# Kernel tuning notes

Hardware: AMD Instinct MI355X
Metric: run time of the kernel (lower is better)

## Reference

```python
import jax, jax.numpy as jnp
import numpy as np

N = 50000      # batch_node_num (unique nodes)
E = 800000     # number of edges (avg degree 16)
IN = 128       # in_dim
OUT = 128      # out_dim
B = 10000      # query nodes


def setup_inputs() -> dict:
    key = jax.random.key(0)
    k = jax.random.split(key, 8)
    edges = jax.random.randint(k[0], (E, 2), 0, N, dtype=jnp.int64)
    node_idx = jax.random.randint(k[1], (B,), 0, N, dtype=jnp.int64)
    local_features = jax.random.normal(k[2], (N, IN), dtype=jnp.float32)
    W1 = jax.random.normal(k[3], (IN, OUT), dtype=jnp.float32) * (1.0 / np.sqrt(IN))
    b1 = jnp.zeros((OUT,), dtype=jnp.float32)
    W2 = jax.random.normal(k[4], (OUT, OUT), dtype=jnp.float32) * (1.0 / np.sqrt(OUT))
    b2 = jnp.zeros((OUT,), dtype=jnp.float32)
    return {"edges": edges, "node_idx": node_idx, "local_features": local_features,
            "W1": W1, "b1": b1, "W2": W2, "b2": b2, "ind": 2}


def reference(edges, node_idx, local_features, W1, b1, W2, b2, ind):
    mask = jnp.array([1.0, 1.0, 0.0, 0.0], dtype=jnp.float32)
    # Linear -> Tanh -> Linear (the out_linear_layer MLP)
    h = jnp.tanh(local_features @ W1 + b1) @ W2 + b2          # [N, OUT]
    src, dst = edges[:, 0], edges[:, 1]
    # self-loop edges get weight mask[ind], others weight 1
    values = jnp.where(src == dst, mask[ind], jnp.float32(1.0))  # [E]
    # spmm(matrix, ones) == per-row degree (weighted)
    row_sum = jax.ops.segment_sum(values, src, num_segments=N)   # [N]
    row_sum = jnp.where(row_sum == 0, jnp.float32(1.0), row_sum)
    # spmm(matrix, new_embeddings): gather dst embeddings, scatter-add to src
    results = jax.ops.segment_sum(values[:, None] * h[dst], src, num_segments=N)  # [N, OUT]
    output_emb = results / row_sum[:, None]
    return output_emb[node_idx]
```

## Files before the change

kernel.cpp:

```cpp
#include <hip/hip_runtime.h>

#define IN_DIM 128
#define CAP 128
#define LDT 136
#define SCAT_BLOCKS 377

typedef short v8s __attribute__((ext_vector_type(8)));
typedef float v4f __attribute__((ext_vector_type(4)));

__device__ inline unsigned short f2bf(float f) {
    unsigned int u = __float_as_uint(f);
    u += 0x7FFFu + ((u >> 16) & 1u);
    return (unsigned short)(u >> 16);
}
__device__ inline float bf2f(unsigned short h) {
    return __uint_as_float((unsigned int)h << 16);
}
__device__ inline float fast_tanh(float x) {
    float e = __builtin_amdgcn_exp2f(x * 2.885390081777927f);
    return 1.0f - 2.0f * __builtin_amdgcn_rcpf(e + 1.0f);
}

__global__ __launch_bounds__(256) void prep(
    const float* __restrict__ W1, const float* __restrict__ W2,
    unsigned short* __restrict__ Wf1, unsigned short* __restrict__ Wf2,
    const int* __restrict__ node_idx, int* __restrict__ flag, int B,
    int* __restrict__ cursor, int N, int nbF)
{
    int bid = blockIdx.x;
    if (bid < 128) {
        int i = bid * 256 + threadIdx.x;
        int m = i >> 14, o = i & 16383;
        int j   = o & 7;
        int l15 = (o >> 3) & 15;
        int quad = (o >> 7) & 3;
        int ct  = (o >> 9) & 7;
        int kk  = (o >> 12) & 3;
        int k = kk * 32 + quad * 8 + j;
        int n = ct * 16 + l15;
        float wv = (m ? W2 : W1)[k * 128 + n];
        (m ? Wf2 : Wf1)[o] = f2bf(wv);
    } else if (bid < 128 + nbF) {
        int i = (bid - 128) * 256 + threadIdx.x;
        if (i < B) flag[node_idx[i]] = 1;
    } else {
        int i = (bid - 128 - nbF) * 256 + threadIdx.x;
        if (i < N) cursor[i] = 0;
    }
}

__global__ __launch_bounds__(256, 3) void mlp_fill(
    const float* __restrict__ X,
    const unsigned short* __restrict__ Wf1, const unsigned short* __restrict__ Wf2,
    const float* __restrict__ b1, const float* __restrict__ b2,
    unsigned short* __restrict__ Hb, int nrows,
    const int* __restrict__ edges, const int* __restrict__ flag,
    const int* __restrict__ indp, int* __restrict__ cursor,
    unsigned short* __restrict__ col, int E, int mlpBlocks)
{
    const int bid = blockIdx.x;

    if (bid >= mlpBlocks) {
        const int keepSelf = (*indp < 2) ? 1 : 0;
        const int stride = SCAT_BLOCKS * 256;
        for (int e = (bid - mlpBlocks) * 256 + threadIdx.x; e < E; e += stride) {
            int2 ed = ((const int2*)edges)[e];
            if ((ed.x != ed.y || keepSelf) && flag[ed.x] == 1) {
                int p = atomicAdd(&cursor[ed.x], 1);
                if (p < CAP)
                    col[(size_t)ed.x * CAP + p] = (unsigned short)ed.y;
            }
        }
        return;
    }

    __shared__ unsigned short Ts[4 * 32 * LDT];
    const int t    = threadIdx.x;
    const int w    = t >> 6;
    const int lane = t & 63;
    const int l15  = lane & 15;
    const int quad = lane >> 4;
    const int R0   = bid * 128;
    const int wrow = w * 32;
    unsigned short* Tw = &Ts[w * 32 * LDT];

    int gr0 = R0 + wrow + l15;        gr0 = gr0 < nrows ? gr0 : nrows - 1;
    int gr1 = R0 + wrow + 16 + l15;   gr1 = gr1 < nrows ? gr1 : nrows - 1;
    const float* xrow[2] = { &X[(size_t)gr0 * 128 + quad * 8],
                             &X[(size_t)gr1 * 128 + quad * 8] };

    const v8s* Wp1 = (const v8s*)Wf1 + lane;
    const v8s* Wp2 = (const v8s*)Wf2 + lane;

    v4f acc[2][8];
#pragma unroll
    for (int rt = 0; rt < 2; ++rt)
#pragma unroll
        for (int ct = 0; ct < 8; ++ct)
            acc[rt][ct] = (v4f){0.f, 0.f, 0.f, 0.f};

#pragma unroll
    for (int kk = 0; kk < 4; ++kk) {
        v8s Ar[2];
#pragma unroll
        for (int rt = 0; rt < 2; ++rt) {
            const float* xp = xrow[rt] + kk * 32;
            float4 x0 = *(const float4*)xp;
            float4 x1 = *(const float4*)(xp + 4);
            v8s av;
            av[0] = (short)f2bf(x0.x); av[1] = (short)f2bf(x0.y);
            av[2] = (short)f2bf(x0.z); av[3] = (short)f2bf(x0.w);
            av[4] = (short)f2bf(x1.x); av[5] = (short)f2bf(x1.y);
            av[6] = (short)f2bf(x1.z); av[7] = (short)f2bf(x1.w);
            Ar[rt] = av;
        }
#pragma unroll
        for (int ct = 0; ct < 8; ++ct) {
            v8s Bfc = Wp1[(kk * 8 + ct) * 64];
            acc[0][ct] = __builtin_amdgcn_mfma_f32_16x16x32_bf16(
                Ar[0], Bfc, acc[0][ct], 0, 0, 0);
            acc[1][ct] = __builtin_amdgcn_mfma_f32_16x16x32_bf16(
                Ar[1], Bfc, acc[1][ct], 0, 0, 0);
        }
    }
#pragma unroll
    for (int ct = 0; ct < 8; ++ct) {
        float bias = b1[ct * 16 + l15];
#pragma unroll
        for (int rt = 0; rt < 2; ++rt) {
#pragma unroll
            for (int r = 0; r < 4; ++r)
                Tw[(rt * 16 + quad * 4 + r) * LDT + ct * 16 + l15] =
                    f2bf(fast_tanh(acc[rt][ct][r] + bias));
            acc[rt][ct] = (v4f){0.f, 0.f, 0.f, 0.f};
        }
    }


#pragma unroll
    for (int kk = 0; kk < 4; ++kk) {
        v8s Ar[2];
#pragma unroll
        for (int rt = 0; rt < 2; ++rt)
            Ar[rt] = *(const v8s*)
                &Tw[(rt * 16 + l15) * LDT + kk * 32 + quad * 8];
#pragma unroll
        for (int ct = 0; ct < 8; ++ct) {
            v8s Bfc = Wp2[(kk * 8 + ct) * 64];
            acc[0][ct] = __builtin_amdgcn_mfma_f32_16x16x32_bf16(
                Ar[0], Bfc, acc[0][ct], 0, 0, 0);
            acc[1][ct] = __builtin_amdgcn_mfma_f32_16x16x32_bf16(
                Ar[1], Bfc, acc[1][ct], 0, 0, 0);
        }
    }
    asm volatile("s_waitcnt lgkmcnt(0)" ::: "memory");
#pragma unroll
    for (int ct = 0; ct < 8; ++ct) {
        float bias = b2[ct * 16 + l15];
#pragma unroll
        for (int rt = 0; rt < 2; ++rt)
#pragma unroll
            for (int r = 0; r < 4; ++r)
                Tw[(rt * 16 + quad * 4 + r) * LDT + ct * 16 + l15] =
                    f2bf(acc[rt][ct][r] + bias);
    }
    asm volatile("s_waitcnt lgkmcnt(0)" ::: "memory");
#pragma unroll
    for (int i = 0; i < 8; ++i) {
        int lr = i * 4 + quad;
        int c  = l15;
        uint4 v = *(const uint4*)&Tw[lr * LDT + c * 8];
        int grow = R0 + wrow + lr;
        if (grow < nrows)
            *(uint4*)&Hb[(size_t)grow * 128 + c * 8] = v;
    }
}

__global__ __launch_bounds__(256) void aggregate_out(
    const int* __restrict__ node_idx, const int* __restrict__ cursor,
    const unsigned short* __restrict__ col, const unsigned short* __restrict__ Hb,
    float* __restrict__ out, int B)
{
    int b = (int)((blockIdx.x * blockDim.x + threadIdx.x) >> 6);
    if (b >= B) return;
    int lane = threadIdx.x & 63;
    int v = __builtin_amdgcn_readfirstlane(node_idx[b]);
    int deg = cursor[v];
    deg = deg < CAP ? deg : CAP;
    const unsigned short* cp = &col[(size_t)v * CAP];

    float sx[4] = {0.f, 0.f, 0.f, 0.f};
    float sy[4] = {0.f, 0.f, 0.f, 0.f};
    for (int c0 = 0; c0 < deg; c0 += 16) {
        unsigned int u[16];
#pragma unroll
        for (int k = 0; k < 16; ++k) {
            int idx = c0 + k;
            idx = idx < deg ? idx : deg - 1;
            int d = (int)cp[idx];
            u[k] = *(const unsigned int*)&Hb[(size_t)d * 128 + lane * 2];
        }
        int dn = deg - c0;
#pragma unroll
        for (int k = 0; k < 16; ++k) {
            unsigned int uv = (k < dn) ? u[k] : 0u;
            sx[k & 3] += bf2f((unsigned short)(uv & 0xFFFFu));
            sy[k & 3] += bf2f((unsigned short)(uv >> 16));
        }
    }
    float den = (deg > 0) ? (float)deg : 1.0f;
    float ox = ((sx[0] + sx[1]) + (sx[2] + sx[3])) / den;
    float oy = ((sy[0] + sy[1]) + (sy[2] + sy[3])) / den;
    *(float2*)&out[(size_t)b * 128 + lane * 2] = make_float2(ox, oy);
}

extern "C" void kernel_launch(void* const* d_in, const int* in_sizes, int n_in,
                              void* d_out, int out_size, void* d_ws, size_t ws_size,
                              hipStream_t stream)
{
    const int*   edges    = (const int*)d_in[0];
    const int*   node_idx = (const int*)d_in[1];
    const float* X        = (const float*)d_in[2];
    const float* W1       = (const float*)d_in[3];
    const float* b1       = (const float*)d_in[4];
    const float* W2       = (const float*)d_in[5];
    const float* b2       = (const float*)d_in[6];
    const int*   indp     = (const int*)d_in[7];

    const int E = in_sizes[0] / 2;
    const int B = in_sizes[1];
    const int N = in_sizes[2] / IN_DIM;
    const int mlpBlocks = (N + 127) / 128;
    const int nbF = (B + 255) / 256;
    const int nbC = (N + 255) / 256;

    char* ws = (char*)d_ws;
    size_t off = 0;
    int* cursor = (int*)(ws + off); off += (size_t)N * 4;
    int* flag   = (int*)(ws + off); off += (size_t)N * 4;
    off = (off + 15) & ~(size_t)15;
    unsigned short* Hb  = (unsigned short*)(ws + off); off += (size_t)N * IN_DIM * 2;
    unsigned short* col = (unsigned short*)(ws + off); off += (size_t)N * CAP * 2;
    unsigned short* Wf1 = (unsigned short*)(ws + off); off += 16384 * 2;
    unsigned short* Wf2 = (unsigned short*)(ws + off); off += 16384 * 2;

    hipLaunchKernelGGL(prep, dim3(128 + nbF + nbC), dim3(256), 0, stream,
                       W1, W2, Wf1, Wf2, node_idx, flag, B, cursor, N, nbF);
    hipLaunchKernelGGL(mlp_fill, dim3(mlpBlocks + SCAT_BLOCKS), dim3(256),
                       0, stream, X, Wf1, Wf2, b1, b2, Hb, N,
                       edges, flag, indp, cursor, col, E, mlpBlocks);
    hipLaunchKernelGGL(aggregate_out, dim3((B * 64 + 255) / 256), dim3(256), 0,
                       stream, node_idx, cursor, col, Hb, (float*)d_out, B);
}
```

Measured before the change: 110.3 us.

## Use node bitmask for query flags and 16-byte gathers in aggregation

Replaces the per-node int flag array with a bitmask built in shared memory by a single block, so the edge-filter loop reads a much smaller structure that stays in cache. This also fixes the old flag array never being cleared between calls. The aggregation kernel now has each wavefront process four neighbours at once, with each lane loading 16 bytes instead of 4, and combines the four partial sums with cross-lane shuffles. The costs are a serial single-block bitmask build over all B query nodes, a shared array hardcoded to 2048 words (N up to 65536), and the shuffle reductions.

```diff
diff --git a/kernel.cpp b/kernel.cpp
--- a/kernel.cpp
+++ b/kernel.cpp
@@ -24,8 +24,8 @@
 __global__ __launch_bounds__(256) void prep(
     const float* __restrict__ W1, const float* __restrict__ W2,
     unsigned short* __restrict__ Wf1, unsigned short* __restrict__ Wf2,
-    const int* __restrict__ node_idx, int* __restrict__ flag, int B,
-    int* __restrict__ cursor, int N, int nbF)
+    const int* __restrict__ node_idx, unsigned int* __restrict__ bits, int B,
+    int* __restrict__ cursor, int N)
 {
     int bid = blockIdx.x;
     if (bid < 128) {
@@ -40,11 +40,19 @@
         int n = ct * 16 + l15;
         float wv = (m ? W2 : W1)[k * 128 + n];
         (m ? Wf2 : Wf1)[o] = f2bf(wv);
-    } else if (bid < 128 + nbF) {
-        int i = (bid - 128) * 256 + threadIdx.x;
-        if (i < B) flag[node_idx[i]] = 1;
+    } else if (bid == 128) {
+        __shared__ unsigned int lbits[2048];
+        int nb = (N + 31) >> 5;
+        for (int i = threadIdx.x; i < nb; i += 256) lbits[i] = 0u;
+        __syncthreads();
+        for (int i = threadIdx.x; i < B; i += 256) {
+            int v = node_idx[i];
+            atomicOr(&lbits[v >> 5], 1u << (v & 31));
+        }
+        __syncthreads();
+        for (int i = threadIdx.x; i < nb; i += 256) bits[i] = lbits[i];
     } else {
-        int i = (bid - 128 - nbF) * 256 + threadIdx.x;
+        int i = (bid - 129) * 256 + threadIdx.x;
         if (i < N) cursor[i] = 0;
     }
 }
@@ -54,7 +62,7 @@
     const unsigned short* __restrict__ Wf1, const unsigned short* __restrict__ Wf2,
     const float* __restrict__ b1, const float* __restrict__ b2,
     unsigned short* __restrict__ Hb, int nrows,
-    const int* __restrict__ edges, const int* __restrict__ flag,
+    const int* __restrict__ edges, const unsigned int* __restrict__ bits,
     const int* __restrict__ indp, int* __restrict__ cursor,
     unsigned short* __restrict__ col, int E, int mlpBlocks)
 {
@@ -65,7 +73,8 @@
         const int stride = SCAT_BLOCKS * 256;
         for (int e = (bid - mlpBlocks) * 256 + threadIdx.x; e < E; e += stride) {
             int2 ed = ((const int2*)edges)[e];
-            if ((ed.x != ed.y || keepSelf) && flag[ed.x] == 1) {
+            unsigned int bw = bits[ed.x >> 5];
+            if ((ed.x != ed.y || keepSelf) && ((bw >> (ed.x & 31)) & 1u)) {
                 int p = atomicAdd(&cursor[ed.x], 1);
                 if (p < CAP)
                     col[(size_t)ed.x * CAP + p] = (unsigned short)ed.y;
@@ -184,34 +193,52 @@
     int b = (int)((blockIdx.x * blockDim.x + threadIdx.x) >> 6);
     if (b >= B) return;
     int lane = threadIdx.x & 63;
+    int rg   = lane >> 4;
+    int c16  = lane & 15;
     int v = __builtin_amdgcn_readfirstlane(node_idx[b]);
     int deg = cursor[v];
     deg = deg < CAP ? deg : CAP;
     const unsigned short* cp = &col[(size_t)v * CAP];
 
-    float sx[4] = {0.f, 0.f, 0.f, 0.f};
-    float sy[4] = {0.f, 0.f, 0.f, 0.f};
+    float s[8] = {0.f, 0.f, 0.f, 0.f, 0.f, 0.f, 0.f, 0.f};
     for (int c0 = 0; c0 < deg; c0 += 16) {
-        unsigned int u[16];
-#pragma unroll
-        for (int k = 0; k < 16; ++k) {
-            int idx = c0 + k;
+        uint4 u[4];
+#pragma unroll
+        for (int q = 0; q < 4; ++q) {
+            int idx = c0 + q * 4 + rg;
             idx = idx < deg ? idx : deg - 1;
             int d = (int)cp[idx];
-            u[k] = *(const unsigned int*)&Hb[(size_t)d * 128 + lane * 2];
-        }
-        int dn = deg - c0;
-#pragma unroll
-        for (int k = 0; k < 16; ++k) {
-            unsigned int uv = (k < dn) ? u[k] : 0u;
-            sx[k & 3] += bf2f((unsigned short)(uv & 0xFFFFu));
-            sy[k & 3] += bf2f((unsigned short)(uv >> 16));
-        }
-    }
-    float den = (deg > 0) ? (float)deg : 1.0f;
-    float ox = ((sx[0] + sx[1]) + (sx[2] + sx[3])) / den;
-    float oy = ((sy[0] + sy[1]) + (sy[2] + sy[3])) / den;
-    *(float2*)&out[(size_t)b * 128 + lane * 2] = make_float2(ox, oy);
+            u[q] = *(const uint4*)&Hb[(size_t)d * 128 + c16 * 8];
+        }
+#pragma unroll
+        for (int q = 0; q < 4; ++q) {
+            bool ok = (c0 + q * 4 + rg) < deg;
+            unsigned int w0 = ok ? u[q].x : 0u;
+            unsigned int w1 = ok ? u[q].y : 0u;
+            unsigned int w2 = ok ? u[q].z : 0u;
+            unsigned int w3 = ok ? u[q].w : 0u;
+            s[0] += bf2f((unsigned short)(w0 & 0xFFFFu));
+            s[1] += bf2f((unsigned short)(w0 >> 16));
+            s[2] += bf2f((unsigned short)(w1 & 0xFFFFu));
+            s[3] += bf2f((unsigned short)(w1 >> 16));
+            s[4] += bf2f((unsigned short)(w2 & 0xFFFFu));
+            s[5] += bf2f((unsigned short)(w2 >> 16));
+            s[6] += bf2f((unsigned short)(w3 & 0xFFFFu));
+            s[7] += bf2f((unsigned short)(w3 >> 16));
+        }
+    }
+#pragma unroll
+    for (int k = 0; k < 8; ++k) {
+        s[k] += __shfl_xor(s[k], 16, 64);
+        s[k] += __shfl_xor(s[k], 32, 64);
+    }
+    if (rg == 0) {
+        float den = (deg > 0) ? (float)deg : 1.0f;
+        float4 o0 = make_float4(s[0] / den, s[1] / den, s[2] / den, s[3] / den);
+        float4 o1 = make_float4(s[4] / den, s[5] / den, s[6] / den, s[7] / den);
+        *(float4*)&out[(size_t)b * 128 + c16 * 8]     = o0;
+        *(float4*)&out[(size_t)b * 128 + c16 * 8 + 4] = o1;
+    }
 }
 
 extern "C" void kernel_launch(void* const* d_in, const int* in_sizes, int n_in,
@@ -231,24 +258,23 @@
     const int B = in_sizes[1];
     const int N = in_sizes[2] / IN_DIM;
     const int mlpBlocks = (N + 127) / 128;
-    const int nbF = (B + 255) / 256;
     const int nbC = (N + 255) / 256;
 
     char* ws = (char*)d_ws;
     size_t off = 0;
-    int* cursor = (int*)(ws + off); off += (size_t)N * 4;
-    int* flag   = (int*)(ws + off); off += (size_t)N * 4;
+    int*          cursor = (int*)(ws + off);          off += (size_t)N * 4;
+    unsigned int* bits   = (unsigned int*)(ws + off); off += (size_t)((N + 31) / 32) * 4;
     off = (off + 15) & ~(size_t)15;
     unsigned short* Hb  = (unsigned short*)(ws + off); off += (size_t)N * IN_DIM * 2;
     unsigned short* col = (unsigned short*)(ws + off); off += (size_t)N * CAP * 2;
     unsigned short* Wf1 = (unsigned short*)(ws + off); off += 16384 * 2;
     unsigned short* Wf2 = (unsigned short*)(ws + off); off += 16384 * 2;
 
-    hipLaunchKernelGGL(prep, dim3(128 + nbF + nbC), dim3(256), 0, stream,
-                       W1, W2, Wf1, Wf2, node_idx, flag, B, cursor, N, nbF);
+    hipLaunchKernelGGL(prep, dim3(129 + nbC), dim3(256), 0, stream,
+                       W1, W2, Wf1, Wf2, node_idx, bits, B, cursor, N);
     hipLaunchKernelGGL(mlp_fill, dim3(mlpBlocks + SCAT_BLOCKS), dim3(256),
                        0, stream, X, Wf1, Wf2, b1, b2, Hb, N,
-                       edges, flag, indp, cursor, col, E, mlpBlocks);
+                       edges, bits, indp, cursor, col, E, mlpBlocks);
     hipLaunchKernelGGL(aggregate_out, dim3((B * 64 + 255) / 256), dim3(256), 0,
                        stream, node_idx, cursor, col, Hb, (float*)d_out, B);
 }
```

After: 122.4 us. 1.11x slower.
